# Kernel tuning notes

Measured on AMD Instinct MI355X. Metric: run time of the kernel, lower is better.

## Reference

```python
import jax, jax.numpy as jnp
import numpy as np

T = 4096        # teams (HC nodes)
N_COORD = 3     # coordinators per team (OC, SC, DC)
N_POS = 32      # position coaches per coordinator
NPT = 1 + N_COORD + N_COORD * N_POS   # 100 nodes per team
N = T * NPT     # 409600 total nodes
IN_DIM = 128
EMB = 64


def _build_indices():
    base = np.arange(T, dtype=np.int32) * NPT
    hc_ids = base                                                    # [T]
    coord = base[:, None] + 1 + np.arange(N_COORD, dtype=np.int32)   # [T,3]
    pos = (base[:, None, None] + 1 + N_COORD
           + (np.arange(N_COORD, dtype=np.int32) * N_POS)[None, :, None]
           + np.arange(N_POS, dtype=np.int32)[None, None, :])        # [T,3,32]
    src1 = np.broadcast_to(coord[:, :, None], (T, N_COORD, N_POS)).reshape(-1)
    tgt1 = pos.reshape(-1)
    src2 = np.repeat(base, N_COORD)
    tgt2 = coord.reshape(-1)
    return (jnp.asarray(src1), jnp.asarray(tgt1),
            jnp.asarray(src2), jnp.asarray(tgt2), jnp.asarray(hc_ids))


def setup_inputs() -> dict:
    key = jax.random.key(0)
    k = jax.random.split(key, 5)
    src1, tgt1, src2, tgt2, hc_ids = _build_indices()
    gain = 1.414  # relu gain, xavier_normal-style scale
    f = jax.random.normal(k[0], (N, IN_DIM), jnp.float32)
    salary = jax.random.normal(k[1], (T, 1), jnp.float32)
    W_fc = jax.random.normal(k[2], (EMB, IN_DIM), jnp.float32) * gain * (2.0 / (IN_DIM + EMB)) ** 0.5
    W_attn = jax.random.normal(k[3], (1, 2 * EMB), jnp.float32) * gain * (2.0 / (2 * EMB + 1)) ** 0.5
    b_attn = jnp.zeros((1,), jnp.float32)
    W_out = jax.random.normal(k[4], (2, EMB + 1), jnp.float32) * gain * (2.0 / (EMB + 1 + 2)) ** 0.5
    b_out = jnp.zeros((2,), jnp.float32)
    return {"f": f, "salary": salary, "W_fc": W_fc, "W_attn": W_attn,
            "b_attn": b_attn, "W_out": W_out, "b_out": b_out,
            "src1": src1, "tgt1": tgt1, "src2": src2, "tgt2": tgt2,
            "hc_ids": hc_ids}


def _segment_softmax(e, seg, num_segments):
    m = jax.ops.segment_max(e, seg, num_segments=num_segments)
    ex = jnp.exp(e - m[seg])
    denom = jax.ops.segment_sum(ex, seg, num_segments=num_segments)
    return ex / denom[seg]


def _gat_level(z, src, tgt, W_attn, b_attn):
    # per-edge attention logit: leaky_relu(attn_fc([z_src, z_tgt]))
    z2 = jnp.concatenate([z[src], z[tgt]], axis=1)          # [E, 2*EMB]
    e = jax.nn.leaky_relu(z2 @ W_attn.T + b_attn)[:, 0]     # [E]
    alpha = _segment_softmax(e, src, N)                     # softmax over edges grouped by source
    agg = jax.ops.segment_sum(alpha[:, None] * z[tgt], src, num_segments=N)
    has_edge = jax.ops.segment_sum(jnp.ones_like(e), src, num_segments=N) > 0
    # only source nodes get their z replaced by relu(weighted sum)
    return jnp.where(has_edge[:, None], jax.nn.relu(agg), z)


def reference(f, salary, W_fc, W_attn, b_attn, W_out, b_out,
              src1, tgt1, src2, tgt2, hc_ids):
    z = jax.nn.relu(f @ W_fc.T)                             # [N, EMB]
    z = _gat_level(z, src1, tgt1, W_attn, b_attn)           # coord <- positions
    z = _gat_level(z, src2, tgt2, W_attn, b_attn)           # hc <- coords
    team_emb = z[hc_ids]                                    # [T, EMB]
    h = jnp.concatenate([team_emb, salary], axis=1)         # [T, EMB+1]
    y = jax.nn.relu(h @ W_out.T + b_out)                    # [T, 2]
    return jax.nn.softmax(y, axis=1)
```

## Files before the change

### kernel.cpp

```cpp
#include <hip/hip_runtime.h>

typedef short v8s __attribute__((ext_vector_type(8)));
typedef float v4f __attribute__((ext_vector_type(4)));
typedef unsigned int v4u __attribute__((ext_vector_type(4)));

#define NPT 100
#define IN_DIM 128

__device__ __forceinline__ unsigned int cvt_pk(float x0, float x1) {
    unsigned int r;
    asm("v_cvt_pk_bf16_f32 %0, %1, %2" : "=v"(r) : "v"(x0), "v"(x1));
    return r;
}
__device__ __forceinline__ float bflo(unsigned int u) { return __uint_as_float(u << 16); }
__device__ __forceinline__ float bfhi(unsigned int u) { return __uint_as_float(u & 0xffff0000u); }

union ABfrag { v8s v; v4u u; };

__device__ __forceinline__ ABfrag pack8(float4 x0, float4 x1) {
    ABfrag r;
    r.u[0] = cvt_pk(x0.x, x0.y);
    r.u[1] = cvt_pk(x0.z, x0.w);
    r.u[2] = cvt_pk(x1.x, x1.y);
    r.u[3] = cvt_pk(x1.z, x1.w);
    return r;
}

#define ISSUE(BUF, FP, T) do {                                                   \
    int r_ = 16 * (T) + l15; if (r_ > NPT - 1) r_ = NPT - 1;                     \
    const float* rp_ = (FP) + r_ * IN_DIM + 8 * g;                               \
    _Pragma("unroll") for (int ks_ = 0; ks_ < 4; ++ks_) {                        \
        BUF[ks_][0] = *(const float4*)(rp_ + ks_ * 32);                          \
        BUF[ks_][1] = *(const float4*)(rp_ + ks_ * 32 + 4);                      \
    }                                                                            \
} while (0)

#define CONSUME(T, BUF) do {                                                     \
    v4f acc_[4] = {{0,0,0,0},{0,0,0,0},{0,0,0,0},{0,0,0,0}};                     \
    _Pragma("unroll") for (int ks_ = 0; ks_ < 4; ++ks_) {                        \
        ABfrag fr_ = pack8(BUF[ks_][0], BUF[ks_][1]);                            \
        _Pragma("unroll") for (int n_ = 0; n_ < 4; ++n_) {                       \
            v8s bh_ = *(const v8s*)&wl[(ks_ * 256 + n_ * 64 + lane) * 8];        \
            acc_[n_] = __builtin_amdgcn_mfma_f32_16x16x32_bf16(fr_.v, bh_, acc_[n_], 0, 0, 0); \
        }                                                                        \
    }                                                                            \
    float zr_[4][4];                                                             \
    _Pragma("unroll") for (int n_ = 0; n_ < 4; ++n_)                             \
        _Pragma("unroll") for (int j_ = 0; j_ < 4; ++j_)                         \
            zr_[n_][j_] = fmaxf(acc_[n_][j_], 0.f);                              \
    _Pragma("unroll") for (int n_ = 0; n_ < 4; ++n_) {                           \
        zp[T][n_][0] = cvt_pk(zr_[n_][0], zr_[n_][1]);                           \
        zp[T][n_][1] = cvt_pk(zr_[n_][2], zr_[n_][3]);                           \
    }                                                                            \
    const bool useL_ = ((T) == 0) && (g == 0);            \
    _Pragma("unroll") for (int j_ = 0; j_ < 4; ++j_) {                           \
        float d_ = (useL_ ? aLv[0] : aRv[0]) * zr_[0][j_]                        \
                 + (useL_ ? aLv[1] : aRv[1]) * zr_[1][j_]                        \
                 + (useL_ ? aLv[2] : aRv[2]) * zr_[2][j_]                        \
                 + (useL_ ? aLv[3] : aRv[3]) * zr_[3][j_];                       \
        d_ += __shfl_xor(d_, 8, 64); d_ += __shfl_xor(d_, 4, 64);                \
        d_ += __shfl_xor(d_, 2, 64); d_ += __shfl_xor(d_, 1, 64);                \
        const int r_ = 16 * (T) + 4 * g + j_;                                    \
        if (l15 == j_ && ((T) < 6 || r_ < NPT)) sDa[r_] = d_;                    \
    }                                                                            \
} while (0)

#define TAIL(TEAMI) do {                                                         \
    {                       \
        const int c_ = lane >> 5, p_ = lane & 31;                                \
        float e_ = sDa[1 + c_] + sDa[4 + 32 * c_ + p_] + bA;                     \
        e_ = e_ > 0.f ? e_ : 0.01f * e_;                                         \
        float mx_ = e_;                                                          \
        mx_ = fmaxf(mx_, __shfl_xor(mx_, 16, 64)); mx_ = fmaxf(mx_, __shfl_xor(mx_, 8, 64)); \
        mx_ = fmaxf(mx_, __shfl_xor(mx_, 4, 64));  mx_ = fmaxf(mx_, __shfl_xor(mx_, 2, 64)); \
        mx_ = fmaxf(mx_, __shfl_xor(mx_, 1, 64));                                \
        float ex_ = __expf(e_ - mx_), sm_ = ex_;                                 \
        sm_ += __shfl_xor(sm_, 16, 64); sm_ += __shfl_xor(sm_, 8, 64);           \
        sm_ += __shfl_xor(sm_, 4, 64);  sm_ += __shfl_xor(sm_, 2, 64);           \
        sm_ += __shfl_xor(sm_, 1, 64);                                           \
        sDa[4 + lane] = ex_ / sm_;                                               \
    }                                                                            \
    if (lane < 32) {                                                \
        float e_ = sDa[3] + sDa[68 + lane] + bA;                                 \
        e_ = e_ > 0.f ? e_ : 0.01f * e_;                                         \
        float mx_ = e_;                                                          \
        mx_ = fmaxf(mx_, __shfl_xor(mx_, 16, 64)); mx_ = fmaxf(mx_, __shfl_xor(mx_, 8, 64)); \
        mx_ = fmaxf(mx_, __shfl_xor(mx_, 4, 64));  mx_ = fmaxf(mx_, __shfl_xor(mx_, 2, 64)); \
        mx_ = fmaxf(mx_, __shfl_xor(mx_, 1, 64));                                \
        float ex_ = __expf(e_ - mx_), sm_ = ex_;                                 \
        sm_ += __shfl_xor(sm_, 16, 64); sm_ += __shfl_xor(sm_, 8, 64);           \
        sm_ += __shfl_xor(sm_, 4, 64);  sm_ += __shfl_xor(sm_, 2, 64);           \
        sm_ += __shfl_xor(sm_, 1, 64);                                           \
        sDa[68 + lane] = ex_ / sm_;                                              \
    }                                                                            \
     \
     \
    float zn_[3][4], sRn_[3];                                                    \
    _Pragma("unroll") for (int c_ = 0; c_ < 3; ++c_) {                           \
        float s_[4] = {0.f, 0.f, 0.f, 0.f};                                      \
        _Pragma("unroll") for (int ti_ = 0; ti_ < 3; ++ti_) {                    \
            const int T_ = 2 * c_ + ti_;                                         \
            float4 av_ = *(const float4*)&sDa[16 * T_ + 4 * g];                  \
            const float msk_ = (ti_ == 0) ? (g >= 1 ? 1.f : 0.f)                 \
                             : (ti_ == 2) ? (g == 0 ? 1.f : 0.f) : 1.f;          \
            av_.x *= msk_; av_.y *= msk_; av_.z *= msk_; av_.w *= msk_;          \
            _Pragma("unroll") for (int n_ = 0; n_ < 4; ++n_) {                   \
                s_[n_] += av_.x * bflo(zp[T_][n_][0]) + av_.y * bfhi(zp[T_][n_][0]) \
                        + av_.z * bflo(zp[T_][n_][1]) + av_.w * bfhi(zp[T_][n_][1]); \
            }                                                                    \
        }                                                                        \
        _Pragma("unroll") for (int n_ = 0; n_ < 4; ++n_) {                       \
            s_[n_] += __shfl_xor(s_[n_], 16, 64);                                \
            s_[n_] += __shfl_xor(s_[n_], 32, 64);                                \
            zn_[c_][n_] = fmaxf(s_[n_], 0.f);                                    \
        }                                                                        \
        float pr_ = aRv[0] * zn_[c_][0] + aRv[1] * zn_[c_][1]                    \
                  + aRv[2] * zn_[c_][2] + aRv[3] * zn_[c_][3];                   \
        pr_ += __shfl_xor(pr_, 8, 64); pr_ += __shfl_xor(pr_, 4, 64);            \
        pr_ += __shfl_xor(pr_, 2, 64); pr_ += __shfl_xor(pr_, 1, 64);            \
        sRn_[c_] = pr_;                                                          \
    }                                                                            \
    {                                                     \
        const float s0_ = sDa[0];                                                \
        float e0_ = s0_ + sRn_[0] + bA; e0_ = e0_ > 0.f ? e0_ : 0.01f * e0_;     \
        float e1_ = s0_ + sRn_[1] + bA; e1_ = e1_ > 0.f ? e1_ : 0.01f * e1_;     \
        float e2_ = s0_ + sRn_[2] + bA; e2_ = e2_ > 0.f ? e2_ : 0.01f * e2_;     \
        const float mx_ = fmaxf(e0_, fmaxf(e1_, e2_));                           \
        const float x0_ = __expf(e0_ - mx_), x1_ = __expf(e1_ - mx_), x2_ = __expf(e2_ - mx_); \
        const float inv_ = 1.f / (x0_ + x1_ + x2_);                              \
        float p0_ = 0.f, p1_ = 0.f;                                              \
        _Pragma("unroll") for (int n_ = 0; n_ < 4; ++n_) {                       \
            const float zh_ = fmaxf((x0_ * zn_[0][n_] + x1_ * zn_[1][n_]         \
                                   + x2_ * zn_[2][n_]) * inv_, 0.f);             \
            p0_ += W_out[n_ * 16 + l15] * zh_;                                   \
            p1_ += W_out[65 + n_ * 16 + l15] * zh_;                              \
        }                                                                        \
        p0_ += __shfl_xor(p0_, 8, 64); p0_ += __shfl_xor(p0_, 4, 64);            \
        p0_ += __shfl_xor(p0_, 2, 64); p0_ += __shfl_xor(p0_, 1, 64);            \
        p1_ += __shfl_xor(p1_, 8, 64); p1_ += __shfl_xor(p1_, 4, 64);            \
        p1_ += __shfl_xor(p1_, 2, 64); p1_ += __shfl_xor(p1_, 1, 64);            \
        if (lane == 0) {                                                         \
            const float sal_ = salary[TEAMI];                                    \
            float y0_ = fmaxf(p0_ + W_out[64]  * sal_ + b_out[0], 0.f);          \
            float y1_ = fmaxf(p1_ + W_out[129] * sal_ + b_out[1], 0.f);          \
            const float mm_ = fmaxf(y0_, y1_);                                   \
            const float q0_ = __expf(y0_ - mm_), q1_ = __expf(y1_ - mm_);        \
            const float is_ = 1.f / (q0_ + q1_);                                 \
            out[(TEAMI) * 2 + 0] = q0_ * is_;                                    \
            out[(TEAMI) * 2 + 1] = q1_ * is_;                                    \
        }                                                                        \
    }                                                                            \
} while (0)

__global__ __launch_bounds__(256, 4) void wteam1_kernel(
    const float* __restrict__ f, const float* __restrict__ salary,
    const float* __restrict__ W_fc, const float* __restrict__ W_attn,
    const float* __restrict__ b_attn, const float* __restrict__ W_out,
    const float* __restrict__ b_out, float* __restrict__ out)
{
    __shared__ __align__(16) unsigned short wl[8192];
    __shared__ __align__(16) float sD_all[4][112];

    const int tid  = threadIdx.x;
    const int lane = tid & 63;
    const int wave = tid >> 6;
    const int l15  = lane & 15;
    const int g    = lane >> 4;
    float* sDa = sD_all[wave];

    #pragma unroll
    for (int i = 0; i < 4; ++i) {
        const int s = i * 256 + tid;
        const int ks = s >> 8, nt = (s >> 6) & 3, sl = s & 63;
        const float* src = W_fc + (nt * 16 + (sl & 15)) * IN_DIM + ks * 32 + 8 * (sl >> 4);
        ABfrag wv = pack8(*(const float4*)src, *(const float4*)(src + 4));
        *(v4u*)&wl[s * 8] = wv.u;
    }

    float aLv[4], aRv[4];
    #pragma unroll
    for (int n = 0; n < 4; ++n) {
        aLv[n] = W_attn[n * 16 + l15];
        aRv[n] = W_attn[64 + n * 16 + l15];
    }
    const float bA = b_attn[0];

    const size_t team = (size_t)blockIdx.x * 4 + wave;
    const float* f0 = f + team * (NPT * IN_DIM);

    __syncthreads();

    float4 buf[4][2];
    unsigned int zp[7][4][2];

    ISSUE(buf, f0, 0);
    CONSUME(0, buf); ISSUE(buf, f0, 1);
    CONSUME(1, buf); ISSUE(buf, f0, 2);
    CONSUME(2, buf); ISSUE(buf, f0, 3);
    CONSUME(3, buf); ISSUE(buf, f0, 4);
    CONSUME(4, buf); ISSUE(buf, f0, 5);
    CONSUME(5, buf); ISSUE(buf, f0, 6);
    CONSUME(6, buf);
    TAIL(team);
}

extern "C" void kernel_launch(void* const* d_in, const int* in_sizes, int n_in,
                              void* d_out, int out_size, void* d_ws, size_t ws_size,
                              hipStream_t stream) {
    const float* f      = (const float*)d_in[0];
    const float* salary = (const float*)d_in[1];
    const float* W_fc   = (const float*)d_in[2];
    const float* W_attn = (const float*)d_in[3];
    const float* b_attn = (const float*)d_in[4];
    const float* W_out  = (const float*)d_in[5];
    const float* b_out  = (const float*)d_in[6];
    wteam1_kernel<<<dim3(1024), dim3(256), 0, stream>>>(
        f, salary, W_fc, W_attn, b_attn, W_out, b_out, (float*)d_out);
}
```

Measured before the change: 45.37 us.

## Stream team features through swizzled LDS double buffer, two teams per wave

```diff
diff --git a/kernel.cpp b/kernel.cpp
--- a/kernel.cpp
+++ b/kernel.cpp
@@ -3,9 +3,11 @@
 typedef short v8s __attribute__((ext_vector_type(8)));
 typedef float v4f __attribute__((ext_vector_type(4)));
 typedef unsigned int v4u __attribute__((ext_vector_type(4)));
+typedef unsigned int v2u __attribute__((ext_vector_type(2)));
 
 #define NPT 100
 #define IN_DIM 128
+#define FMAXO 209715184u
 
 __device__ __forceinline__ unsigned int cvt_pk(float x0, float x1) {
     unsigned int r;
@@ -26,28 +28,42 @@
     return r;
 }
 
-#define ISSUE(BUF, FP, T) do {                                                   \
-    int r_ = 16 * (T) + l15; if (r_ > NPT - 1) r_ = NPT - 1;                     \
-    const float* rp_ = (FP) + r_ * IN_DIM + 8 * g;                               \
-    _Pragma("unroll") for (int ks_ = 0; ks_ < 4; ++ks_) {                        \
-        BUF[ks_][0] = *(const float4*)(rp_ + ks_ * 32);                          \
-        BUF[ks_][1] = *(const float4*)(rp_ + ks_ * 32 + 4);                      \
-    }                                                                            \
-} while (0)
-
-#define CONSUME(T, BUF) do {                                                     \
+#define ISSUE(BUF, TBOFF) do {                                                   \
+    _Pragma("unroll") for (int i_ = 0; i_ < 8; ++i_) {                           \
+        unsigned o_ = (TBOFF) + i_ * 1024u + lane16;                             \
+        o_ = o_ < FMAXO ? o_ : FMAXO;                                            \
+        BUF[i_] = *(const v4f*)(fbytes + o_);                                    \
+    }                                                                            \
+} while (0)
+
+#define TSTORE(LT, BUF) do {                                                     \
+    _Pragma("unroll") for (int i_ = 0; i_ < 8; ++i_) {                           \
+        const int row_ = 2 * i_ + (lane >> 5);                                   \
+        unsigned b_ = (unsigned)(row_ * 256 + (lane & 31) * 8);                  \
+        b_ ^= (unsigned)((row_ & 7) << 4);                                       \
+        v2u w_;                                                                  \
+        w_.x = cvt_pk(BUF[i_].x, BUF[i_].y);                                     \
+        w_.y = cvt_pk(BUF[i_].z, BUF[i_].w);                                     \
+        *(v2u*)((LT) + b_) = w_;                                                 \
+    }                                                                            \
+} while (0)
+
+#define CONSUME(T, LT) do {                                                      \
     v4f acc_[4] = {{0,0,0,0},{0,0,0,0},{0,0,0,0},{0,0,0,0}};                     \
     _Pragma("unroll") for (int ks_ = 0; ks_ < 4; ++ks_) {                        \
-        ABfrag fr_ = pack8(BUF[ks_][0], BUF[ks_][1]);                            \
+        const unsigned rb_ = (unsigned)(l15 * 256 + ks_ * 64 + g * 16)           \
+                           ^ (unsigned)((l15 & 7) << 4);                         \
+        v8s fr_ = *(const v8s*)((LT) + rb_);                                     \
         _Pragma("unroll") for (int n_ = 0; n_ < 4; ++n_) {                       \
             v8s bh_ = *(const v8s*)&wl[(ks_ * 256 + n_ * 64 + lane) * 8];        \
-            acc_[n_] = __builtin_amdgcn_mfma_f32_16x16x32_bf16(fr_.v, bh_, acc_[n_], 0, 0, 0); \
-        }                                                                        \
-    }                                                                            \
+            acc_[n_] = __builtin_amdgcn_mfma_f32_16x16x32_bf16(fr_, bh_, acc_[n_], 0, 0, 0); \
+        }                                                                        \
+    }                                                                            \
+    const bool live_ = ((T) < 6) || (g == 0);                                    \
     float zr_[4][4];                                                             \
     _Pragma("unroll") for (int n_ = 0; n_ < 4; ++n_)                             \
         _Pragma("unroll") for (int j_ = 0; j_ < 4; ++j_)                         \
-            zr_[n_][j_] = fmaxf(acc_[n_][j_], 0.f);                              \
+            zr_[n_][j_] = live_ ? fmaxf(acc_[n_][j_], 0.f) : 0.f;                \
     _Pragma("unroll") for (int n_ = 0; n_ < 4; ++n_) {                           \
         zp[T][n_][0] = cvt_pk(zr_[n_][0], zr_[n_][1]);                           \
         zp[T][n_][1] = cvt_pk(zr_[n_][2], zr_[n_][3]);                           \
@@ -93,8 +109,6 @@
         sm_ += __shfl_xor(sm_, 1, 64);                                           \
         sDa[68 + lane] = ex_ / sm_;                                              \
     }                                                                            \
-     \
-     \
     float zn_[3][4], sRn_[3];                                                    \
     _Pragma("unroll") for (int c_ = 0; c_ < 3; ++c_) {                           \
         float s_[4] = {0.f, 0.f, 0.f, 0.f};                                      \
@@ -120,7 +134,7 @@
         pr_ += __shfl_xor(pr_, 2, 64); pr_ += __shfl_xor(pr_, 1, 64);            \
         sRn_[c_] = pr_;                                                          \
     }                                                                            \
-    {                                                     \
+    {                                                                            \
         const float s0_ = sDa[0];                                                \
         float e0_ = s0_ + sRn_[0] + bA; e0_ = e0_ > 0.f ? e0_ : 0.01f * e0_;     \
         float e1_ = s0_ + sRn_[1] + bA; e1_ = e1_ > 0.f ? e1_ : 0.01f * e1_;     \
@@ -152,13 +166,14 @@
     }                                                                            \
 } while (0)
 
-__global__ __launch_bounds__(256, 4) void wteam1_kernel(
+__global__ __launch_bounds__(256, 2) void wteam2_kernel(
     const float* __restrict__ f, const float* __restrict__ salary,
     const float* __restrict__ W_fc, const float* __restrict__ W_attn,
     const float* __restrict__ b_attn, const float* __restrict__ W_out,
     const float* __restrict__ b_out, float* __restrict__ out)
 {
     __shared__ __align__(16) unsigned short wl[8192];
+    __shared__ __align__(16) char lt_all[4][2][4096];
     __shared__ __align__(16) float sD_all[4][112];
 
     const int tid  = threadIdx.x;
@@ -166,7 +181,11 @@
     const int wave = tid >> 6;
     const int l15  = lane & 15;
     const int g    = lane >> 4;
+    const unsigned lane16 = (unsigned)lane * 16u;
     float* sDa = sD_all[wave];
+    char* LT0 = lt_all[wave][0];
+    char* LT1 = lt_all[wave][1];
+    const char* fbytes = (const char*)f;
 
     #pragma unroll
     for (int i = 0; i < 4; ++i) {
@@ -184,24 +203,36 @@
         aRv[n] = W_attn[64 + n * 16 + l15];
     }
     const float bA = b_attn[0];
-
-    const size_t team = (size_t)blockIdx.x * 4 + wave;
-    const float* f0 = f + team * (NPT * IN_DIM);
+    if (lane < 12) sDa[100 + lane] = 0.f;
+
+    const size_t team0 = ((size_t)blockIdx.x * 4 + wave) * 2;
+    const unsigned tb0 = (unsigned)team0 * 51200u;
+    const unsigned tb1 = tb0 + 51200u;
 
     __syncthreads();
 
-    float4 buf[4][2];
+    v4f R0[8], R1[8];
     unsigned int zp[7][4][2];
 
-    ISSUE(buf, f0, 0);
-    CONSUME(0, buf); ISSUE(buf, f0, 1);
-    CONSUME(1, buf); ISSUE(buf, f0, 2);
-    CONSUME(2, buf); ISSUE(buf, f0, 3);
-    CONSUME(3, buf); ISSUE(buf, f0, 4);
-    CONSUME(4, buf); ISSUE(buf, f0, 5);
-    CONSUME(5, buf); ISSUE(buf, f0, 6);
-    CONSUME(6, buf);
-    TAIL(team);
+    ISSUE(R0, tb0 + 0 * 8192u);
+    ISSUE(R1, tb0 + 1 * 8192u);
+    TSTORE(LT0, R0);
+    ISSUE(R0, tb0 + 2 * 8192u); TSTORE(LT1, R1); CONSUME(0, LT0);
+    ISSUE(R1, tb0 + 3 * 8192u); TSTORE(LT0, R0); CONSUME(1, LT1);
+    ISSUE(R0, tb0 + 4 * 8192u); TSTORE(LT1, R1); CONSUME(2, LT0);
+    ISSUE(R1, tb0 + 5 * 8192u); TSTORE(LT0, R0); CONSUME(3, LT1);
+    ISSUE(R0, tb0 + 6 * 8192u); TSTORE(LT1, R1); CONSUME(4, LT0);
+    ISSUE(R1, tb1 + 0 * 8192u); TSTORE(LT0, R0); CONSUME(5, LT1);
+    ISSUE(R0, tb1 + 1 * 8192u); TSTORE(LT1, R1); CONSUME(6, LT0);
+    TAIL(team0);
+    ISSUE(R1, tb1 + 2 * 8192u); TSTORE(LT0, R0); CONSUME(0, LT1);
+    ISSUE(R0, tb1 + 3 * 8192u); TSTORE(LT1, R1); CONSUME(1, LT0);
+    ISSUE(R1, tb1 + 4 * 8192u); TSTORE(LT0, R0); CONSUME(2, LT1);
+    ISSUE(R0, tb1 + 5 * 8192u); TSTORE(LT1, R1); CONSUME(3, LT0);
+    ISSUE(R1, tb1 + 6 * 8192u); TSTORE(LT0, R0); CONSUME(4, LT1);
+    TSTORE(LT1, R1); CONSUME(5, LT0);
+    CONSUME(6, LT1);
+    TAIL(team0 + 1);
 }
 
 extern "C" void kernel_launch(void* const* d_in, const int* in_sizes, int n_in,
@@ -214,6 +245,6 @@
     const float* b_attn = (const float*)d_in[4];
     const float* W_out  = (const float*)d_in[5];
     const float* b_out  = (const float*)d_in[6];
-    wteam1_kernel<<<dim3(1024), dim3(256), 0, stream>>>(
+    wteam2_kernel<<<dim3(512), dim3(256), 0, stream>>>(
         f, salary, W_fc, W_attn, b_attn, W_out, b_out, (float*)d_out);
 }
```

Measured after the change: 42.72 us, median of 2. 1.06x faster.
